# Kernel tuning notes

Measured on AMD Instinct MI355X. Metric: run time of the kernel, lower is better.

The kernel has to match this reference:

```python
import jax, jax.numpy as jnp
import numpy as np

N = 100_000      # nodes
E = 3_200_000    # edges
F_IN = 9
F_HID = 9
F_OUT = 1
EPS = 1e-5

def _ln(x, g, b):
    m = x.mean(-1, keepdims=True)
    v = x.var(-1, keepdims=True)
    return (x - m) / jnp.sqrt(v + EPS) * g + b

def _gat(x, src, dst, edge_attr, W, a_src, a_dst, We, a_e, bias):
    # Single-head GATConv with edge_dim=1, add_self_loops=True, fill_value='mean'
    n = x.shape[0]
    loop = jnp.arange(n)
    deg = jax.ops.segment_sum(jnp.ones((src.shape[0],), x.dtype), dst, n)
    loop_attr = jax.ops.segment_sum(edge_attr, dst, n) / jnp.maximum(deg, 1.0)[:, None]
    s = jnp.concatenate([src, loop])
    d = jnp.concatenate([dst, loop])
    ea = jnp.concatenate([edge_attr, loop_attr], axis=0)   # [E+N, 1]
    xp = x @ W                                             # [N, C]
    a = (xp * a_src).sum(-1)[s] + (xp * a_dst).sum(-1)[d] + ((ea @ We) * a_e).sum(-1)
    a = jax.nn.leaky_relu(a, 0.2)
    amax = jax.ops.segment_max(a, d, n)
    aexp = jnp.exp(a - amax[d])
    denom = jax.ops.segment_sum(aexp, d, n)
    alpha = aexp / (denom[d] + 1e-16)
    return jax.ops.segment_sum(alpha[:, None] * xp[s], d, n) + bias

def setup_inputs() -> dict:
    key = jax.random.key(0)
    ks = jax.random.split(key, 16)
    def rn(k, shp, s):
        return jax.random.normal(k, shp, jnp.float32) * s
    return {
        "x": jax.random.normal(ks[0], (N, F_IN), jnp.float32),
        "edge_index": jax.random.randint(ks[1], (2, E), 0, N, jnp.int32),
        "edge_attr": jax.random.normal(ks[2], (E, 1), jnp.float32),
        "ln1_g": jnp.ones((F_IN,), jnp.float32), "ln1_b": jnp.zeros((F_IN,), jnp.float32),
        "W0": rn(ks[3], (F_IN, F_HID), 0.3), "as0": rn(ks[4], (F_HID,), 0.3),
        "ad0": rn(ks[5], (F_HID,), 0.3), "We0": rn(ks[6], (1, F_HID), 0.3),
        "ae0": rn(ks[7], (F_HID,), 0.3), "b0": jnp.zeros((F_HID,), jnp.float32),
        "W1": rn(ks[8], (F_HID, F_HID), 0.3), "as1": rn(ks[9], (F_HID,), 0.3),
        "ad1": rn(ks[10], (F_HID,), 0.3), "We1": rn(ks[11], (1, F_HID), 0.3),
        "ae1": rn(ks[12], (F_HID,), 0.3), "b1": jnp.zeros((F_HID,), jnp.float32),
        "ng1": jnp.ones((F_HID,), jnp.float32), "nb1": jnp.zeros((F_HID,), jnp.float32),
        "ln2_g": jnp.ones((2 * F_HID,), jnp.float32), "ln2_b": jnp.zeros((2 * F_HID,), jnp.float32),
        "et_W": rn(ks[13], (2 * F_HID, F_HID), 0.2), "et_b": jnp.zeros((F_HID,), jnp.float32),
        "fc_W": rn(ks[14], (F_HID, F_OUT), 0.3), "fc_b": jnp.zeros((F_OUT,), jnp.float32),
        "att_W": rn(ks[15], (2 * F_OUT, F_OUT), 0.5), "att_b": jnp.zeros((F_OUT,), jnp.float32),
    }

def reference(x, edge_index, edge_attr, ln1_g, ln1_b, W0, as0, ad0, We0, ae0, b0,
              W1, as1, ad1, We1, ae1, b1, ng1, nb1, ln2_g, ln2_b,
              et_W, et_b, fc_W, fc_b, att_W, att_b):
    src, dst = edge_index[0], edge_index[1]
    h = _ln(x, ln1_g, ln1_b)
    # layer 0: no norm/residual
    h = jax.nn.leaky_relu(_gat(h, src, dst, edge_attr, W0, as0, ad0, We0, ae0, b0), 0.01)
    # layer 1: norm + residual
    ident = h
    h = _ln(_gat(h, src, dst, edge_attr, W1, as1, ad1, We1, ae1, b1), ng1, nb1) + ident
    h = jax.nn.leaky_relu(h, 0.01)
    # edge path: gather-concat-norm-MLP  [E, 2H]
    ef = _ln(jnp.concatenate([h[src], h[dst]], axis=1), ln2_g, ln2_b)
    eo = jax.nn.leaky_relu(ef @ et_W + et_b, 0.01)
    eo = eo @ fc_W + fc_b                       # [E, 1]
    # AttentionLayer
    comb = jnp.concatenate([eo, edge_attr], axis=1)   # [E, 2]
    w = jax.nn.softmax(comb @ att_W + att_b, axis=-1) # [E, 1]
    att = (w * comb).sum(axis=1, keepdims=True)       # [E, 1]
    return att + eo
```

## Files before the change

### kernel.cpp

```cpp
#include <hip/hip_runtime.h>
#include <hip/hip_bf16.h>
#include <hip/hip_fp16.h>

typedef __hip_bfloat16 bf16;
typedef unsigned int uint;
typedef unsigned short ushort;
#define TPB 256
#define TPBS 1024
#define TPBG 512
#define BSH 7
#define BNODES 128
#define NBK_MAX 1024
#define CH 8192
#define CAP 4608

enum {
  LN1G = 0, LN1B = 9, PW0 = 18, AS0 = 99, AD0 = 108, CE0 = 117, B0 = 118,
  PW1 = 127, AS1 = 208, AD1 = 217, CE1 = 226, B1 = 227, NG = 236, NB = 245,
  LN2G = 254, LN2B = 272, ETW = 290, ETB = 452, FCW = 461, FCB = 470,
  GC = 471, KC = 480, NPARAM = 489
};

static __device__ __forceinline__ float lrelu(float x, float s) { return x >= 0.f ? x : s * x; }
static __device__ __forceinline__ float ldx(const void* p, long i, int isb) {
    return isb ? __bfloat162float(((const bf16*)p)[i]) : ((const float*)p)[i];
}
static __device__ __forceinline__ uint bfb(float f) {
    uint u = __float_as_uint(f);
    return (u + 0x7FFFu + ((u >> 16) & 1u)) >> 16;
}
static __device__ __forceinline__ uint pack2(float a, float b) { return bfb(a) | (bfb(b) << 16); }
static __device__ __forceinline__ float unlo(uint u) { return __uint_as_float(u << 16); }
static __device__ __forceinline__ float unhi(uint u) { return __uint_as_float(u & 0xFFFF0000u); }
static __device__ __forceinline__ ushort h16(float f) { return __half_as_ushort(__float2half(f)); }
static __device__ __forceinline__ uint p2h(float a, float b) { return (uint)h16(a) | ((uint)h16(b) << 16); }
static __device__ __forceinline__ float hfl(uint u) { return __half2float(__ushort_as_half((ushort)(u & 0xFFFFu))); }
static __device__ __forceinline__ float hfh(uint u) { return __half2float(__ushort_as_half((ushort)(u >> 16))); }
static __device__ __forceinline__ float hfs(ushort u) { return __half2float(__ushort_as_half(u)); }

__global__ void k_params(const void* ln1g, const void* ln1b,
                         const void* W0, const void* as0, const void* ad0,
                         const void* We0, const void* ae0, const void* b0,
                         const void* W1, const void* as1, const void* ad1,
                         const void* We1, const void* ae1, const void* b1,
                         const void* ng, const void* nb,
                         const void* ln2g, const void* ln2b,
                         const void* etW, const void* etb,
                         const void* fcW, const void* fcb,
                         float* __restrict__ P, int* __restrict__ flagp,
                         int* __restrict__ gcursor, int nbk)
{
    __shared__ int sflag;
    if (threadIdx.x == 0) {
        unsigned short h0 = ((const unsigned short*)ln1g)[0];
        sflag = (h0 == 0x3F80u) ? 1 : 0;
        *flagp = sflag;
    }
    __syncthreads();
    const int f = sflag;
    const int t = threadIdx.x;
    for (int j = t; j < nbk; j += TPB) gcursor[j] = j * CAP;
    for (int i = t; i < 9; i += TPB) {
        P[LN1G + i] = ldx(ln1g, i, f); P[LN1B + i] = ldx(ln1b, i, f);
        P[AS0 + i] = ldx(as0, i, f);   P[AD0 + i] = ldx(ad0, i, f);
        P[B0 + i]  = ldx(b0, i, f);
        P[AS1 + i] = ldx(as1, i, f);   P[AD1 + i] = ldx(ad1, i, f);
        P[B1 + i]  = ldx(b1, i, f);
        P[NG + i]  = ldx(ng, i, f);    P[NB + i]  = ldx(nb, i, f);
        P[ETB + i] = ldx(etb, i, f);   P[FCW + i] = ldx(fcW, i, f);
    }
    for (int i = t; i < 81; i += TPB) { P[PW0 + i] = ldx(W0, i, f); P[PW1 + i] = ldx(W1, i, f); }
    for (int i = t; i < 18; i += TPB) { P[LN2G + i] = ldx(ln2g, i, f); P[LN2B + i] = ldx(ln2b, i, f); }
    for (int i = t; i < 162; i += TPB) P[ETW + i] = ldx(etW, i, f) * ldx(ln2g, i / 9, f);
    if (t == 0) {
        float c0 = 0.f, c1 = 0.f;
        for (int k = 0; k < 9; k++) {
            c0 += ldx(We0, k, f) * ldx(ae0, k, f);
            c1 += ldx(We1, k, f) * ldx(ae1, k, f);
        }
        P[CE0] = c0; P[CE1] = c1; P[FCB] = ldx(fcb, 0, f);
        for (int c = 0; c < 9; c++) {
            float gc = 0.f, kc = 0.f;
            for (int k = 0; k < 18; k++) {
                float wv = ldx(etW, (long)k * 9 + c, f);
                gc += ldx(ln2g, k, f) * wv;
                kc += ldx(ln2b, k, f) * wv;
            }
            P[GC + c] = gc;
            P[KC + c] = kc + ldx(etb, c, f);
        }
    }
}

__global__ void __launch_bounds__(TPBS)
k_bscatter(const int* __restrict__ src, const int* __restrict__ dst,
           const void* __restrict__ ea, const int* __restrict__ flagp,
           int* __restrict__ gcursor, int2* __restrict__ ebuf, int e, int nbk)
{
    __shared__ int cnt[NBK_MAX];
    __shared__ int scn[NBK_MAX];
    __shared__ int base[NBK_MAX];
    __shared__ int cur[NBK_MAX];
    __shared__ uint sidx[CH];
    const int tid = threadIdx.x;
    const int s0 = blockIdx.x * CH;
    const int m = min(e - s0, CH);
    for (int j = tid; j < nbk; j += TPBS) cnt[j] = 0;
    __syncthreads();
    for (int t = tid; t < m; t += TPBS) atomicAdd(&cnt[dst[s0 + t] >> BSH], 1);
    __syncthreads();
    for (int j = tid; j < nbk; j += TPBS) {
        int c = cnt[j];
        base[j] = c ? atomicAdd(&gcursor[j], c) : 0;
    }
    scn[tid] = (tid < nbk) ? cnt[tid] : 0;
    __syncthreads();
    for (int off = 1; off < NBK_MAX; off <<= 1) {
        int v = scn[tid] + (tid >= off ? scn[tid - off] : 0);
        __syncthreads();
        scn[tid] = v;
        __syncthreads();
    }
    if (tid < nbk) cur[tid] = scn[tid] - cnt[tid];
    __syncthreads();
    for (int t = tid; t < m; t += TPBS) {
        int d = dst[s0 + t];
        int b = d >> BSH;
        int slot = atomicAdd(&cur[b], 1);
        sidx[slot] = (uint)t | (((uint)d & (BNODES - 1)) << 13) | ((uint)b << 20);
    }
    __syncthreads();
    const int fl = *flagp;
    for (int j = tid; j < m; j += TPBS) {
        uint u = sidx[j];
        int t = u & 0x1FFF;
        int dl = (u >> 13) & (BNODES - 1);
        int b = u >> 20;
        int excl = scn[b] - cnt[b];
        int pos = base[b] + (j - excl);
        if (pos < (b + 1) * CAP) {
            float eav = ldx(ea, s0 + t, fl);
            ebuf[pos] = make_int2(src[s0 + t] | (dl << 17), __float_as_int(eav));
        }
    }
}

__global__ void k_prep(const void* __restrict__ x, const float* __restrict__ P,
                       const int* __restrict__ flagp,
                       uint* __restrict__ xpb0, float* __restrict__ sd0, int n)
{
    const int fl = *flagp;
    int i = blockIdx.x * blockDim.x + threadIdx.x;
    if (i >= n) return;
    float h[9]; float m = 0.f;
    #pragma unroll
    for (int f = 0; f < 9; f++) { h[f] = ldx(x, (long)i * 9 + f, fl); m += h[f]; }
    m *= (1.f / 9.f);
    float v = 0.f;
    #pragma unroll
    for (int f = 0; f < 9; f++) { float d = h[f] - m; v += d * d; }
    float r = rsqrtf(v * (1.f / 9.f) + 1e-5f);
    #pragma unroll
    for (int f = 0; f < 9; f++) h[f] = (h[f] - m) * r * P[LN1G + f] + P[LN1B + f];
    float xr[9]; float ss = 0.f, sd = 0.f;
    #pragma unroll
    for (int c = 0; c < 9; c++) {
        float acc = 0.f;
        #pragma unroll
        for (int f = 0; f < 9; f++) acc += h[f] * P[PW0 + f * 9 + c];
        xr[c] = acc;
        ss += acc * P[AS0 + c]; sd += acc * P[AD0 + c];
    }
    uint* row = xpb0 + (size_t)i * 8;
    ((uint4*)row)[0] = make_uint4(pack2(xr[0], xr[1]), pack2(xr[2], xr[3]),
                                  pack2(xr[4], xr[5]), pack2(xr[6], xr[7]));
    ((uint4*)row)[1] = make_uint4(pack2(xr[8], ss), 0u, 0u, 0u);
    sd0[i] = sd;
}

__global__ void __launch_bounds__(TPBG)
k_sortg0(const int* __restrict__ gcursor, const int2* __restrict__ ebuf,
         const float* __restrict__ P,
         const uint* __restrict__ xpb0, const float* __restrict__ sd0,
         float* __restrict__ h1, uint* __restrict__ xpb1,
         float* __restrict__ sd1, float* __restrict__ la, int n)
{
    __shared__ int2 seb[CAP];
    __shared__ ushort sidx[CAP];
    __shared__ int hist[BNODES], scn[BNODES], cur[BNODES];
    const int b = blockIdx.x, tid = threadIdx.x;
    const int beg = b * CAP;
    int cnt = gcursor[b] - beg;
    if (cnt > CAP) cnt = CAP;
    if (cnt < 0) cnt = 0;
    for (int j = tid; j < BNODES; j += TPBG) hist[j] = 0;
    __syncthreads();
    for (int j = tid; j < cnt; j += TPBG) {
        int2 v = ebuf[beg + j];
        seb[j] = v;
        atomicAdd(&hist[(v.x >> 17) & (BNODES - 1)], 1);
    }
    __syncthreads();
    if (tid < BNODES) scn[tid] = hist[tid];
    __syncthreads();
    for (int off = 1; off < BNODES; off <<= 1) {
        int v2 = 0;
        if (tid < BNODES) v2 = scn[tid] + (tid >= off ? scn[tid - off] : 0);
        __syncthreads();
        if (tid < BNODES) scn[tid] = v2;
        __syncthreads();
    }
    if (tid < BNODES) cur[tid] = scn[tid] - hist[tid];
    __syncthreads();
    for (int j = tid; j < cnt; j += TPBG) {
        int dl = (seb[j].x >> 17) & (BNODES - 1);
        int slot = atomicAdd(&cur[dl], 1);
        sidx[slot] = (ushort)j;
    }
    __syncthreads();
    const int nd = tid >> 2, l = tid & 3;
    const int i = (b << BSH) + nd;
    if (i < n) {
        const float ce = P[CE0];
        const int locend = scn[nd], locbeg = locend - hist[nd];
        const float sdi = sd0[i];
        float acc[11];
        #pragma unroll
        for (int k = 0; k < 11; k++) acc[k] = 0.f;
        for (int j = locbeg + l; j < locend; j += 4) {
            int2 sl = seb[sidx[j]];
            int s = sl.x & 0x1FFFF;
            float eav = __int_as_float(sl.y);
            const uint* row = xpb0 + (size_t)s * 8;
            uint4 q0 = *(const uint4*)row;
            uint  q2 = row[4];
            float ex = expf(lrelu(unhi(q2) + sdi + ce * eav, 0.2f));
            acc[0] += ex; acc[1] += eav;
            acc[2] += ex * unlo(q0.x); acc[3] += ex * unhi(q0.x);
            acc[4] += ex * unlo(q0.y); acc[5] += ex * unhi(q0.y);
            acc[6] += ex * unlo(q0.z); acc[7] += ex * unhi(q0.z);
            acc[8] += ex * unlo(q0.w); acc[9] += ex * unhi(q0.w);
            acc[10] += ex * unlo(q2);
        }
        #pragma unroll
        for (int k = 0; k < 11; k++) {
            acc[k] += __shfl_xor(acc[k], 1, 64);
            acc[k] += __shfl_xor(acc[k], 2, 64);
        }
        if (l == 0) {
            float denom = acc[0];
            float S[9] = {acc[2], acc[3], acc[4], acc[5], acc[6], acc[7], acc[8], acc[9], acc[10]};
            float deg = (float)hist[nd];
            float lav = acc[1] / fmaxf(deg, 1.f);
            la[i] = lav;
            const uint* row = xpb0 + (size_t)i * 8;
            uint4 q0 = *(const uint4*)row;
            uint  q2 = row[4];
            float o0 = unlo(q0.x), o1 = unhi(q0.x), o2 = unlo(q0.y), o3 = unhi(q0.y);
            float o4 = unlo(q0.z), o5 = unhi(q0.z), o6 = unlo(q0.w), o7 = unhi(q0.w);
            float o8 = unlo(q2),   ssi = unhi(q2);
            float ex0 = expf(lrelu(ssi + sdi + ce * lav, 0.2f));
            denom += ex0;
            S[0] += ex0 * o0; S[1] += ex0 * o1; S[2] += ex0 * o2; S[3] += ex0 * o3;
            S[4] += ex0 * o4; S[5] += ex0 * o5; S[6] += ex0 * o6; S[7] += ex0 * o7;
            S[8] += ex0 * o8;
            float inv = 1.f / (denom + 1e-16f);
            float h[9];
            #pragma unroll
            for (int c = 0; c < 9; c++) h[c] = lrelu(S[c] * inv + P[B0 + c], 0.01f);
            float4* hr = (float4*)(h1 + (size_t)i * 12);
            hr[0] = make_float4(h[0], h[1], h[2], h[3]);
            hr[1] = make_float4(h[4], h[5], h[6], h[7]);
            hr[2] = make_float4(h[8], 0.f, 0.f, 0.f);
            float xr1[9]; float ss2 = 0.f, sd2 = 0.f;
            #pragma unroll
            for (int c = 0; c < 9; c++) {
                float a2 = 0.f;
                #pragma unroll
                for (int f = 0; f < 9; f++) a2 += h[f] * P[PW1 + f * 9 + c];
                xr1[c] = a2;
                ss2 += a2 * P[AS1 + c]; sd2 += a2 * P[AD1 + c];
            }
            uint* rw = xpb1 + (size_t)i * 8;
            ((uint4*)rw)[0] = make_uint4(pack2(xr1[0], xr1[1]), pack2(xr1[2], xr1[3]),
                                         pack2(xr1[4], xr1[5]), pack2(xr1[6], xr1[7]));
            ((uint4*)rw)[1] = make_uint4(pack2(xr1[8], ss2), 0u, 0u, 0u);
            sd1[i] = sd2;
        }
    }
}

__global__ void __launch_bounds__(TPBG)
k_sortg1(const int* __restrict__ gcursor, const int2* __restrict__ ebuf,
         const float* __restrict__ P,
         const uint* __restrict__ xpb1, const float* __restrict__ sd1,
         const float* __restrict__ la, const float* __restrict__ h1,
         uint4* __restrict__ orec, int n)
{
    __shared__ int2 seb[CAP];
    __shared__ ushort sidx[CAP];
    __shared__ int hist[BNODES], scn[BNODES], cur[BNODES];
    const int b = blockIdx.x, tid = threadIdx.x;
    const int beg = b * CAP;
    int cnt = gcursor[b] - beg;
    if (cnt > CAP) cnt = CAP;
    if (cnt < 0) cnt = 0;
    for (int j = tid; j < BNODES; j += TPBG) hist[j] = 0;
    __syncthreads();
    for (int j = tid; j < cnt; j += TPBG) {
        int2 v = ebuf[beg + j];
        seb[j] = v;
        atomicAdd(&hist[(v.x >> 17) & (BNODES - 1)], 1);
    }
    __syncthreads();
    if (tid < BNODES) scn[tid] = hist[tid];
    __syncthreads();
    for (int off = 1; off < BNODES; off <<= 1) {
        int v2 = 0;
        if (tid < BNODES) v2 = scn[tid] + (tid >= off ? scn[tid - off] : 0);
        __syncthreads();
        if (tid < BNODES) scn[tid] = v2;
        __syncthreads();
    }
    if (tid < BNODES) cur[tid] = scn[tid] - hist[tid];
    __syncthreads();
    for (int j = tid; j < cnt; j += TPBG) {
        int dl = (seb[j].x >> 17) & (BNODES - 1);
        int slot = atomicAdd(&cur[dl], 1);
        sidx[slot] = (ushort)j;
    }
    __syncthreads();
    const int nd = tid >> 2, l = tid & 3;
    const int i = (b << BSH) + nd;
    if (i < n) {
        const float ce = P[CE1];
        const int locend = scn[nd], locbeg = locend - hist[nd];
        const float sdi = sd1[i];
        float acc[10];
        #pragma unroll
        for (int k = 0; k < 10; k++) acc[k] = 0.f;
        for (int j = locbeg + l; j < locend; j += 4) {
            int2 sl = seb[sidx[j]];
            int s = sl.x & 0x1FFFF;
            float eav = __int_as_float(sl.y);
            const uint* row = xpb1 + (size_t)s * 8;
            uint4 q0 = *(const uint4*)row;
            uint  q2 = row[4];
            float ex = expf(lrelu(unhi(q2) + sdi + ce * eav, 0.2f));
            acc[0] += ex;
            acc[1] += ex * unlo(q0.x); acc[2] += ex * unhi(q0.x);
            acc[3] += ex * unlo(q0.y); acc[4] += ex * unhi(q0.y);
            acc[5] += ex * unlo(q0.z); acc[6] += ex * unhi(q0.z);
            acc[7] += ex * unlo(q0.w); acc[8] += ex * unhi(q0.w);
            acc[9] += ex * unlo(q2);
        }
        #pragma unroll
        for (int k = 0; k < 10; k++) {
            acc[k] += __shfl_xor(acc[k], 1, 64);
            acc[k] += __shfl_xor(acc[k], 2, 64);
        }
        if (l == 0) {
            float denom = acc[0];
            float S[9] = {acc[1], acc[2], acc[3], acc[4], acc[5], acc[6], acc[7], acc[8], acc[9]};
            const uint* row = xpb1 + (size_t)i * 8;
            uint4 q0 = *(const uint4*)row;
            uint  q2 = row[4];
            float o0 = unlo(q0.x), o1 = unhi(q0.x), o2 = unlo(q0.y), o3 = unhi(q0.y);
            float o4 = unlo(q0.z), o5 = unhi(q0.z), o6 = unlo(q0.w), o7 = unhi(q0.w);
            float o8 = unlo(q2),   ssi = unhi(q2);
            float ex0 = expf(lrelu(ssi + sdi + ce * la[i], 0.2f));
            denom += ex0;
            S[0] += ex0 * o0; S[1] += ex0 * o1; S[2] += ex0 * o2; S[3] += ex0 * o3;
            S[4] += ex0 * o4; S[5] += ex0 * o5; S[6] += ex0 * o6; S[7] += ex0 * o7;
            S[8] += ex0 * o8;
            float inv = 1.f / (denom + 1e-16f);
            float g[9]; float m = 0.f;
            #pragma unroll
            for (int c = 0; c < 9; c++) { g[c] = S[c] * inv + P[B1 + c]; m += g[c]; }
            m *= (1.f / 9.f);
            float v = 0.f;
            #pragma unroll
            for (int c = 0; c < 9; c++) { float d = g[c] - m; v += d * d; }
            float r = rsqrtf(v * (1.f / 9.f) + 1e-5f);
            const float4* hr = (const float4*)(h1 + (size_t)i * 12);
            float4 r0 = hr[0], r1 = hr[1], r2 = hr[2];
            float res[9] = {r0.x, r0.y, r0.z, r0.w, r1.x, r1.y, r1.z, r1.w, r2.x};
            float o[9];
            #pragma unroll
            for (int c = 0; c < 9; c++)
                o[c] = lrelu((g[c] - m) * r * P[NG + c] + P[NB + c] + res[c], 0.01f);
            float psum = 0.f, pss = 0.f;
            #pragma unroll
            for (int c = 0; c < 9; c++) { psum += o[c]; pss += o[c] * o[c]; }
            uint4* rp = orec + (size_t)i * 2;
            rp[0] = make_uint4(p2h(o[0], o[1]), p2h(o[2], o[3]), p2h(o[4], o[5]), p2h(o[6], o[7]));
            rp[1] = make_uint4((uint)h16(o[8]),
                               __float_as_uint(psum * (1.f / 18.f)),
                               __float_as_uint(pss * (1.f / 18.f)), 0u);
        }
    }
}

__global__ void k_edge(const int* __restrict__ src, const int* __restrict__ dst,
                       const void* __restrict__ ea, const float* __restrict__ P,
                       const int* __restrict__ flagp,
                       const uint4* __restrict__ orec, void* __restrict__ outp, int e)
{
    const int fl = *flagp;
    int t = blockIdx.x * blockDim.x + threadIdx.x;
    if (t >= e) return;
    int s = src[t], d = dst[t];
    const uint4* rs = orec + (size_t)s * 2;
    const uint4* rd = orec + (size_t)d * 2;
    uint4 As = rs[0], Bs = rs[1];
    uint4 Ad = rd[0], Bd = rd[1];
    float os[9] = {hfl(As.x), hfh(As.x), hfl(As.y), hfh(As.y),
                   hfl(As.z), hfh(As.z), hfl(As.w), hfh(As.w),
                   hfs((ushort)(Bs.x & 0xFFFFu))};
    float od[9] = {hfl(Ad.x), hfh(Ad.x), hfl(Ad.y), hfh(Ad.y),
                   hfl(Ad.z), hfh(Ad.z), hfl(Ad.w), hfh(Ad.w),
                   hfs((ushort)(Bd.x & 0xFFFFu))};
    float m   = __uint_as_float(Bs.y) + __uint_as_float(Bd.y);
    float ex2 = __uint_as_float(Bs.z) + __uint_as_float(Bd.z);
    float r = rsqrtf(fmaxf(ex2 - m * m, 0.f) + 1e-5f);
    float eo = P[FCB];
    #pragma unroll
    for (int c = 0; c < 9; c++) {
        float dotc = 0.f;
        #pragma unroll
        for (int k = 0; k < 9; k++) {
            dotc = fmaf(os[k], P[ETW + k * 9 + c], dotc);
            dotc = fmaf(od[k], P[ETW + (9 + k) * 9 + c], dotc);
        }
        float pre = fmaf(r, fmaf(-m, P[GC + c], dotc), P[KC + c]);
        float act = fmaxf(pre, 0.01f * pre);
        eo = fmaf(act, P[FCW + c], eo);
    }
    float resv = 2.f * eo + ldx(ea, t, fl);
    if (fl) ((bf16*)outp)[t] = __float2bfloat16(resv);
    else    ((float*)outp)[t] = resv;
}

extern "C" void kernel_launch(void* const* d_in, const int* in_sizes, int n_in,
                              void* d_out, int out_size, void* d_ws, size_t ws_size,
                              hipStream_t stream) {
    const int n = in_sizes[0] / 9;
    const int e = in_sizes[2];
    const int nbk = (n + BNODES - 1) >> BSH;

    const void* X   = d_in[0];
    const int*  ei  = (const int*)d_in[1];
    const int*  src = ei;
    const int*  dst = ei + e;
    const void* EA  = d_in[2];

    char* base = (char*)d_ws;
    size_t off = 0;
    auto alloc = [&](size_t bytes) { void* p = base + off; off += (bytes + 63) & ~size_t(63); return p; };
    float*  P       = (float*)alloc(512 * sizeof(float));
    int*    flagp   = (int*)(P + NPARAM);
    int*    gcursor = (int*)alloc((size_t)NBK_MAX * sizeof(int));
    int2*   ebuf    = (int2*)alloc((size_t)nbk * CAP * sizeof(int2));
    uint*   xpb0    = (uint*)alloc((size_t)n * 8 * sizeof(uint));
    uint*   xpb1    = (uint*)alloc((size_t)n * 8 * sizeof(uint));
    float*  h1      = (float*)alloc((size_t)n * 12 * sizeof(float));
    uint4*  orec    = (uint4*)alloc((size_t)n * 2 * sizeof(uint4));
    float*  sd0     = (float*)alloc((size_t)n * sizeof(float));
    float*  sd1     = (float*)alloc((size_t)n * sizeof(float));
    float*  la      = (float*)alloc((size_t)n * sizeof(float));

    dim3 gN((n + TPB - 1) / TPB);
    dim3 gE((e + TPB - 1) / TPB);
    dim3 gC((e + CH - 1) / CH);
    dim3 gB(nbk);

    k_params<<<1, TPB, 0, stream>>>(d_in[3], d_in[4], d_in[5], d_in[6], d_in[7],
                                    d_in[8], d_in[9], d_in[10], d_in[11], d_in[12],
                                    d_in[13], d_in[14], d_in[15], d_in[16], d_in[17],
                                    d_in[18], d_in[19], d_in[20], d_in[21], d_in[22],
                                    d_in[23], d_in[24], P, flagp, gcursor, nbk);
    k_prep<<<gN, dim3(TPB), 0, stream>>>(X, P, flagp, xpb0, sd0, n);
    k_bscatter<<<gC, dim3(TPBS), 0, stream>>>(src, dst, EA, flagp, gcursor, ebuf, e, nbk);
    k_sortg0<<<gB, dim3(TPBG), 0, stream>>>(gcursor, ebuf, P, xpb0, sd0, h1, xpb1, sd1, la, n);
    k_sortg1<<<gB, dim3(TPBG), 0, stream>>>(gcursor, ebuf, P, xpb1, sd1, la, h1, orec, n);
    k_edge<<<gE, dim3(TPB), 0, stream>>>(src, dst, EA, P, flagp, orec, d_out, e);
}
```

Before: 187.8 us.

## Precompute per-node edge-MLP projections and simplify bucket scatter

The per-edge 18x9 matmul over concatenated endpoint features is factored into two per-node 9-wide projections (source half and destination half, with the LN mean correction folded in). These are computed once per node in k_sortg1 and stored as fp16, so k_edge only adds two gathered vectors before the activation and final dot. Separately, the bucket scatter drops its shared-memory prefix scan and index staging. It caches dst values in registers and claims output slots with per-bucket shared atomics on the global base. This cuts shared memory and barriers, but edge order within a bucket becomes nondeterministic and it adds fp16 rounding of the projected values.

```diff
diff --git a/kernel.cpp b/kernel.cpp
--- a/kernel.cpp
+++ b/kernel.cpp
@@ -6,12 +6,13 @@
 typedef unsigned int uint;
 typedef unsigned short ushort;
 #define TPB 256
-#define TPBS 1024
+#define TPBS 512
 #define TPBG 512
 #define BSH 7
 #define BNODES 128
 #define NBK_MAX 1024
 #define CH 8192
+#define EPT (CH / TPBS)
 #define CAP 4608
 
 enum {
@@ -86,7 +87,7 @@
                 gc += ldx(ln2g, k, f) * wv;
                 kc += ldx(ln2b, k, f) * wv;
             }
-            P[GC + c] = gc;
+            P[GC + c] = gc * (1.f / 18.f);
             P[KC + c] = kc + ldx(etb, c, f);
         }
     }
@@ -98,49 +99,38 @@
            int* __restrict__ gcursor, int2* __restrict__ ebuf, int e, int nbk)
 {
     __shared__ int cnt[NBK_MAX];
-    __shared__ int scn[NBK_MAX];
-    __shared__ int base[NBK_MAX];
     __shared__ int cur[NBK_MAX];
-    __shared__ uint sidx[CH];
     const int tid = threadIdx.x;
     const int s0 = blockIdx.x * CH;
     const int m = min(e - s0, CH);
     for (int j = tid; j < nbk; j += TPBS) cnt[j] = 0;
     __syncthreads();
-    for (int t = tid; t < m; t += TPBS) atomicAdd(&cnt[dst[s0 + t] >> BSH], 1);
+    int dreg[EPT];
+    #pragma unroll
+    for (int k = 0; k < EPT; k++) {
+        int t = tid + k * TPBS;
+        dreg[k] = (t < m) ? dst[s0 + t] : -1;
+        if (t < m) atomicAdd(&cnt[dreg[k] >> BSH], 1);
+    }
     __syncthreads();
     for (int j = tid; j < nbk; j += TPBS) {
         int c = cnt[j];
-        base[j] = c ? atomicAdd(&gcursor[j], c) : 0;
-    }
-    scn[tid] = (tid < nbk) ? cnt[tid] : 0;
-    __syncthreads();
-    for (int off = 1; off < NBK_MAX; off <<= 1) {
-        int v = scn[tid] + (tid >= off ? scn[tid - off] : 0);
-        __syncthreads();
-        scn[tid] = v;
-        __syncthreads();
-    }
-    if (tid < nbk) cur[tid] = scn[tid] - cnt[tid];
-    __syncthreads();
-    for (int t = tid; t < m; t += TPBS) {
-        int d = dst[s0 + t];
-        int b = d >> BSH;
-        int slot = atomicAdd(&cur[b], 1);
-        sidx[slot] = (uint)t | (((uint)d & (BNODES - 1)) << 13) | ((uint)b << 20);
+        cur[j] = c ? atomicAdd(&gcursor[j], c) : 0;
     }
     __syncthreads();
     const int fl = *flagp;
-    for (int j = tid; j < m; j += TPBS) {
-        uint u = sidx[j];
-        int t = u & 0x1FFF;
-        int dl = (u >> 13) & (BNODES - 1);
-        int b = u >> 20;
-        int excl = scn[b] - cnt[b];
-        int pos = base[b] + (j - excl);
-        if (pos < (b + 1) * CAP) {
-            float eav = ldx(ea, s0 + t, fl);
-            ebuf[pos] = make_int2(src[s0 + t] | (dl << 17), __float_as_int(eav));
+    #pragma unroll
+    for (int k = 0; k < EPT; k++) {
+        int t = tid + k * TPBS;
+        if (t < m) {
+            int d = dreg[k];
+            int b = d >> BSH;
+            int pos = atomicAdd(&cur[b], 1);
+            if (pos < (b + 1) * CAP) {
+                float eav = ldx(ea, s0 + t, fl);
+                ebuf[pos] = make_int2(src[s0 + t] | ((d & (BNODES - 1)) << 17),
+                                      __float_as_int(eav));
+            }
         }
     }
 }
@@ -295,7 +285,7 @@
          const float* __restrict__ P,
          const uint* __restrict__ xpb1, const float* __restrict__ sd1,
          const float* __restrict__ la, const float* __restrict__ h1,
-         uint4* __restrict__ orec, int n)
+         uint4* __restrict__ uarr, uint4* __restrict__ warr, int n)
 {
     __shared__ int2 seb[CAP];
     __shared__ ushort sidx[CAP];
@@ -392,47 +382,60 @@
             float psum = 0.f, pss = 0.f;
             #pragma unroll
             for (int c = 0; c < 9; c++) { psum += o[c]; pss += o[c] * o[c]; }
-            uint4* rp = orec + (size_t)i * 2;
-            rp[0] = make_uint4(p2h(o[0], o[1]), p2h(o[2], o[3]), p2h(o[4], o[5]), p2h(o[6], o[7]));
-            rp[1] = make_uint4((uint)h16(o[8]),
-                               __float_as_uint(psum * (1.f / 18.f)),
-                               __float_as_uint(pss * (1.f / 18.f)), 0u);
-        }
-    }
-}
-
-__global__ void k_edge(const int* __restrict__ src, const int* __restrict__ dst,
-                       const void* __restrict__ ea, const float* __restrict__ P,
-                       const int* __restrict__ flagp,
-                       const uint4* __restrict__ orec, void* __restrict__ outp, int e)
+            uint sumb = __float_as_uint(psum * (1.f / 18.f));
+            uint ssb  = __float_as_uint(pss * (1.f / 18.f));
+            float u[9];
+            #pragma unroll
+            for (int c = 0; c < 9; c++) {
+                float a2 = 0.f;
+                #pragma unroll
+                for (int k = 0; k < 9; k++) a2 += o[k] * P[ETW + k * 9 + c];
+                u[c] = a2 - psum * P[GC + c];
+            }
+            uint4* up = uarr + (size_t)i * 2;
+            up[0] = make_uint4(p2h(u[0], u[1]), p2h(u[2], u[3]), p2h(u[4], u[5]), p2h(u[6], u[7]));
+            up[1] = make_uint4((uint)h16(u[8]), sumb, ssb, 0u);
+            #pragma unroll
+            for (int c = 0; c < 9; c++) {
+                float a2 = 0.f;
+                #pragma unroll
+                for (int k = 0; k < 9; k++) a2 += o[k] * P[ETW + (9 + k) * 9 + c];
+                u[c] = a2 - psum * P[GC + c];
+            }
+            uint4* wp = warr + (size_t)i * 2;
+            wp[0] = make_uint4(p2h(u[0], u[1]), p2h(u[2], u[3]), p2h(u[4], u[5]), p2h(u[6], u[7]));
+            wp[1] = make_uint4((uint)h16(u[8]), sumb, ssb, 0u);
+        }
+    }
+}
+
+__global__ void __launch_bounds__(TPB)
+k_edge(const int* __restrict__ src, const int* __restrict__ dst,
+       const void* __restrict__ ea, const float* __restrict__ P,
+       const int* __restrict__ flagp,
+       const uint4* __restrict__ uarr, const uint4* __restrict__ warr,
+       void* __restrict__ outp, int e)
 {
     const int fl = *flagp;
     int t = blockIdx.x * blockDim.x + threadIdx.x;
     if (t >= e) return;
     int s = src[t], d = dst[t];
-    const uint4* rs = orec + (size_t)s * 2;
-    const uint4* rd = orec + (size_t)d * 2;
-    uint4 As = rs[0], Bs = rs[1];
-    uint4 Ad = rd[0], Bd = rd[1];
-    float os[9] = {hfl(As.x), hfh(As.x), hfl(As.y), hfh(As.y),
-                   hfl(As.z), hfh(As.z), hfl(As.w), hfh(As.w),
-                   hfs((ushort)(Bs.x & 0xFFFFu))};
-    float od[9] = {hfl(Ad.x), hfh(Ad.x), hfl(Ad.y), hfh(Ad.y),
-                   hfl(Ad.z), hfh(Ad.z), hfl(Ad.w), hfh(Ad.w),
-                   hfs((ushort)(Bd.x & 0xFFFFu))};
-    float m   = __uint_as_float(Bs.y) + __uint_as_float(Bd.y);
-    float ex2 = __uint_as_float(Bs.z) + __uint_as_float(Bd.z);
+    const uint4* up = uarr + (size_t)s * 2;
+    const uint4* wp = warr + (size_t)d * 2;
+    uint4 a0 = up[0], a1 = up[1];
+    uint4 b0 = wp[0], b1 = wp[1];
+    float m   = __uint_as_float(a1.y) + __uint_as_float(b1.y);
+    float ex2 = __uint_as_float(a1.z) + __uint_as_float(b1.z);
     float r = rsqrtf(fmaxf(ex2 - m * m, 0.f) + 1e-5f);
+    float uv[9] = {hfl(a0.x) + hfl(b0.x), hfh(a0.x) + hfh(b0.x),
+                   hfl(a0.y) + hfl(b0.y), hfh(a0.y) + hfh(b0.y),
+                   hfl(a0.z) + hfl(b0.z), hfh(a0.z) + hfh(b0.z),
+                   hfl(a0.w) + hfl(b0.w), hfh(a0.w) + hfh(b0.w),
+                   hfs((ushort)(a1.x & 0xFFFFu)) + hfs((ushort)(b1.x & 0xFFFFu))};
     float eo = P[FCB];
     #pragma unroll
     for (int c = 0; c < 9; c++) {
-        float dotc = 0.f;
-        #pragma unroll
-        for (int k = 0; k < 9; k++) {
-            dotc = fmaf(os[k], P[ETW + k * 9 + c], dotc);
-            dotc = fmaf(od[k], P[ETW + (9 + k) * 9 + c], dotc);
-        }
-        float pre = fmaf(r, fmaf(-m, P[GC + c], dotc), P[KC + c]);
+        float pre = fmaf(r, uv[c], P[KC + c]);
         float act = fmaxf(pre, 0.01f * pre);
         eo = fmaf(act, P[FCW + c], eo);
     }
@@ -464,7 +467,8 @@
     uint*   xpb0    = (uint*)alloc((size_t)n * 8 * sizeof(uint));
     uint*   xpb1    = (uint*)alloc((size_t)n * 8 * sizeof(uint));
     float*  h1      = (float*)alloc((size_t)n * 12 * sizeof(float));
-    uint4*  orec    = (uint4*)alloc((size_t)n * 2 * sizeof(uint4));
+    uint4*  uarr    = (uint4*)alloc((size_t)n * 2 * sizeof(uint4));
+    uint4*  warr    = (uint4*)alloc((size_t)n * 2 * sizeof(uint4));
     float*  sd0     = (float*)alloc((size_t)n * sizeof(float));
     float*  sd1     = (float*)alloc((size_t)n * sizeof(float));
     float*  la      = (float*)alloc((size_t)n * sizeof(float));
@@ -482,6 +486,6 @@
     k_prep<<<gN, dim3(TPB), 0, stream>>>(X, P, flagp, xpb0, sd0, n);
     k_bscatter<<<gC, dim3(TPBS), 0, stream>>>(src, dst, EA, flagp, gcursor, ebuf, e, nbk);
     k_sortg0<<<gB, dim3(TPBG), 0, stream>>>(gcursor, ebuf, P, xpb0, sd0, h1, xpb1, sd1, la, n);
-    k_sortg1<<<gB, dim3(TPBG), 0, stream>>>(gcursor, ebuf, P, xpb1, sd1, la, h1, orec, n);
-    k_edge<<<gE, dim3(TPB), 0, stream>>>(src, dst, EA, P, flagp, orec, d_out, e);
-}
+    k_sortg1<<<gB, dim3(TPBG), 0, stream>>>(gcursor, ebuf, P, xpb1, sd1, la, h1, uarr, warr, n);
+    k_edge<<<gE, dim3(TPB), 0, stream>>>(src, dst, EA, P, flagp, uarr, warr, d_out, e);
+}
```

Result: slower. 206.8 us (+10.1%).
